# Kernel tuning notes

Hardware: AMD Instinct MI355X
Metric: run time of the kernel (lower is better)

## Reference

```python
import jax, jax.numpy as jnp
import numpy as np

TEMPERATURE = 0.04
EPS = 1e-6

def _conv_valid(x, k, groups=1):
    # x: [N,C,H,W], k: [O,I,kh,kw]
    return jax.lax.conv_general_dilated(
        x, k, window_strides=(1, 1), padding='VALID',
        dimension_numbers=('NCHW', 'OIHW', 'NCHW'),
        feature_group_count=groups)

def setup_inputs() -> dict:
    key = jax.random.key(0)
    k1, k2 = jax.random.split(key)
    roi_piece = jax.random.normal(k1, (256, 1, 17, 17), dtype=jnp.float32)
    roi_background = jax.random.normal(k2, (256, 1, 384, 384), dtype=jnp.float32)
    return {"roi_piece": roi_piece, "roi_background": roi_background}

def reference(roi_piece, roi_background):
    B, _, Ht, Wt = roi_piece.shape
    Hi, Wi = roi_background.shape[-2:]
    Lh, Lw = Hi - Ht + 1, Wi - Wt + 1
    n = Ht * Wt

    # --- template normalization (torch .std is unbiased, ddof=1) ---
    t = roi_piece - jnp.mean(roi_piece, axis=(2, 3), keepdims=True)
    t_std = jnp.maximum(jnp.sqrt(jnp.var(t, axis=(2, 3), keepdims=True, ddof=1)), EPS)
    t_norm = t / t_std  # [B,1,Ht,Wt], zero-mean per batch

    # --- fast ZNCC: since sum(t_norm)==0, corr = corr(image, t_norm) / window_std ---
    # per-batch cross-correlation via grouped conv: batch -> channels/groups
    num = _conv_valid(roi_background.reshape(1, B, Hi, Wi), t_norm, groups=B)[0]  # [B,Lh,Lw]

    # sliding-window mean/var via box filters (var unbiased=False, clamped then sqrt)
    ones_k = jnp.ones((1, 1, Ht, Wt), dtype=roi_background.dtype)
    s1 = _conv_valid(roi_background, ones_k)        # [B,1,Lh,Lw]
    s2 = _conv_valid(roi_background * roi_background, ones_k)
    mu = s1 / n
    var = jnp.maximum(s2 / n - mu * mu, EPS)
    std = jnp.sqrt(var)[:, 0]                        # [B,Lh,Lw]

    corr = num / std  # [B,Lh,Lw]

    # --- soft-argmax over the correlation map ---
    probs = jax.nn.softmax(corr.reshape(B, -1) / TEMPERATURE, axis=-1).reshape(B, Lh, Lw)
    y_coords = jnp.arange(Lh, dtype=corr.dtype)
    x_coords = jnp.arange(Lw, dtype=corr.dtype)
    expected_y = jnp.einsum('bhw,h->b', probs, y_coords)
    expected_x = jnp.einsum('bhw,w->b', probs, x_coords)
    offset_y = expected_y - (Lh - 1) / 2.0
    offset_x = expected_x - (Lw - 1) / 2.0
    offset = jnp.stack([offset_x, offset_y], axis=1)  # [B,2]

    max_corr = jnp.max(corr, axis=(1, 2))             # [B]
    return offset, max_corr
```

## Files before the change

### kernel.cpp

```cpp
#include <hip/hip_runtime.h>
#include <math.h>

#define NB 256
#define HT 17
#define WT 17
#define HI 384
#define WI 384
#define LH 368
#define LW 368
#define NTEMPL 289
#define TPAD 20
#define TY 32
#define TX 128
#define NTXT 3
#define NTYT 12
#define NTILES 36
#define BR 48
#define BP 144
#define TEMP_INV 25.0f
#define EPSV 1e-6f

__global__ __launch_bounds__(256) void tmpl_norm_kernel(
    const float* __restrict__ piece, float* __restrict__ tn) {
    int b = blockIdx.x;
    const float* x = piece + b * NTEMPL;
    int tid = threadIdx.x;
    int wid = tid >> 6, lane = tid & 63;

    float v0 = (tid < NTEMPL) ? x[tid] : 0.f;
    float v1 = (tid + 256 < NTEMPL) ? x[tid + 256] : 0.f;

    __shared__ float sred[4];
    float s = v0 + v1;
    #pragma unroll
    for (int o = 32; o > 0; o >>= 1) s += __shfl_down(s, o, 64);
    if (lane == 0) sred[wid] = s;
    __syncthreads();
    float mean = (sred[0] + sred[1] + sred[2] + sred[3]) * (1.0f / NTEMPL);

    float d0 = (tid < NTEMPL) ? (v0 - mean) : 0.f;
    float d1 = (tid + 256 < NTEMPL) ? (v1 - mean) : 0.f;
    float q = d0 * d0 + d1 * d1;
    __syncthreads();
    #pragma unroll
    for (int o = 32; o > 0; o >>= 1) q += __shfl_down(q, o, 64);
    if (lane == 0) sred[wid] = q;
    __syncthreads();
    float var = (sred[0] + sred[1] + sred[2] + sred[3]) * (1.0f / (NTEMPL - 1));
    float stdv = sqrtf(var);
    if (stdv < EPSV) stdv = EPSV;
    float inv = 1.0f / stdv;

    float* o = tn + b * (HT * TPAD);
    for (int sIdx = tid; sIdx < HT * TPAD; sIdx += 256) {
        int i = sIdx / TPAD, j = sIdx % TPAD;
        o[sIdx] = (j < WT) ? (x[i * WT + j] - mean) * inv : 0.f;
    }
}

template<int P, bool LAST>
__device__ __forceinline__ void corr_step(
    int i, int tr, int xb,
    const float* __restrict__ tp,
    const float (*__restrict__ bg)[BP],
    float (&w)[4][TPAD], float (&tc)[TPAD], float (&acc)[4][4])
{
    const float4* tq = (const float4*)(tp + i * TPAD);
    #pragma unroll
    for (int q = 0; q < 5; ++q) ((float4*)tc)[q] = tq[q];
    #pragma unroll
    for (int j = 0; j < 17; ++j) {
        float tv = tc[j];
        #pragma unroll
        for (int k = 0; k < 4; ++k) acc[0][k] = fmaf(tv, w[P][j + k], acc[0][k]);
    }
    if (!LAST) {
        const float4* br = (const float4*)&bg[tr + i + 4][xb];
        #pragma unroll
        for (int q = 0; q < 5; ++q) ((float4*)w[P])[q] = br[q];
    }
    #pragma unroll
    for (int e = 1; e < 4; ++e) {
        #pragma unroll
        for (int j = 0; j < 17; ++j) {
            float tv = tc[j];
            #pragma unroll
            for (int k = 0; k < 4; ++k)
                acc[e][k] = fmaf(tv, w[(P + e) & 3][j + k], acc[e][k]);
        }
    }
}

template<bool SQ>
__device__ __forceinline__ void build_half(
    const float (*__restrict__ bg)[BP], float (*__restrict__ cb)[BP],
    int r0, int cc)
{
    float s = 0.f;
    #pragma unroll
    for (int i2 = 0; i2 < HT; ++i2) {
        float v = bg[r0 + i2][cc];
        if (SQ) s = fmaf(v, v, s); else s += v;
    }
    cb[0][cc] = s;
    for (int r = 1; r < 16; ++r) {
        float vn = bg[r0 + r + 16][cc], vo = bg[r0 + r - 1][cc];
        if (SQ) s += vn * vn - vo * vo; else s += vn - vo;
        cb[r][cc] = s;
    }
}

__device__ __forceinline__ void consume_half(
    const float (*__restrict__ cb)[BP], int row0, int xb, float (&sv)[4][4])
{
    #pragma unroll
    for (int e = 0; e < 4; ++e) {
        float cf[TPAD];
        const float4* a = (const float4*)&cb[row0 + e][xb];
        #pragma unroll
        for (int q = 0; q < 5; ++q) ((float4*)cf)[q] = a[q];
        float s = 0.f;
        #pragma unroll
        for (int j = 0; j < HT; ++j) s += cf[j];
        sv[e][0] = s;
        #pragma unroll
        for (int k = 1; k < 4; ++k) {
            s += cf[k - 1 + HT] - cf[k - 1];
            sv[e][k] = s;
        }
    }
}

__global__ __launch_bounds__(256, 3) void corr_kernel(
    const float* __restrict__ bgg, const float* __restrict__ tn,
    float* __restrict__ partials) {
    int blk = blockIdx.x;
    int b = blk / NTILES;
    int t = blk % NTILES;
    int ty0 = (t / NTXT) * TY;
    int tx0 = (t % NTXT) * TX;
    const float* img = bgg + (size_t)b * HI * WI;
    const float* tp  = tn + b * (HT * TPAD);

    __shared__ float bg[BR][BP];
    __shared__ float cb[16][BP];
    __shared__ float redm[4], redl[4], redy[4], redx[4];

    int tid = threadIdx.x;
    int wid = tid >> 6, lane = tid & 63;

    for (int l = tid; l < BR * (BP / 4); l += 256) {
        int r = l / (BP / 4), c = (l % (BP / 4)) * 4;
        int iy = ty0 + r, ix = tx0 + c;
        float4 v = make_float4(0.f, 0.f, 0.f, 0.f);
        if (iy < HI && ix < WI) v = *(const float4*)(img + iy * WI + ix);
        *(float4*)&bg[r][c] = v;
    }
    __syncthreads();

    int tr = (tid >> 5) * 4;
    int xb = (tid & 31) * 4;
    float w[4][TPAD];
    float tc[TPAD];
    float acc[4][4] = {};

    #pragma unroll
    for (int m = 0; m < 4; ++m) {
        const float4* br = (const float4*)&bg[tr + m][xb];
        #pragma unroll
        for (int q = 0; q < 5; ++q) ((float4*)w[m])[q] = br[q];
    }

    for (int i = 0; i < 16; i += 4) {
        corr_step<0, false>(i,     tr, xb, tp, bg, w, tc, acc);
        corr_step<1, false>(i + 1, tr, xb, tp, bg, w, tc, acc);
        corr_step<2, false>(i + 2, tr, xb, tp, bg, w, tc, acc);
        corr_step<3, false>(i + 3, tr, xb, tp, bg, w, tc, acc);
    }
    corr_step<0, true>(16, tr, xb, tp, bg, w, tc, acc);

    bool lowHalf = (tr < 16);
    int  row0    = lowHalf ? tr : (tr - 16);
    float s1v[4][4], s2v[4][4];

    if (tid < BP) build_half<false>(bg, cb, 0, tid);
    __syncthreads();
    if (lowHalf) consume_half(cb, row0, xb, s1v);
    __syncthreads();
    if (tid < BP) build_half<false>(bg, cb, 16, tid);
    __syncthreads();
    if (!lowHalf) consume_half(cb, row0, xb, s1v);
    __syncthreads();
    if (tid < BP) build_half<true>(bg, cb, 0, tid);
    __syncthreads();
    if (lowHalf) consume_half(cb, row0, xb, s2v);
    __syncthreads();
    if (tid < BP) build_half<true>(bg, cb, 16, tid);
    __syncthreads();
    if (!lowHalf) consume_half(cb, row0, xb, s2v);

    const float invn = 1.0f / NTEMPL;
    float corr[4][4];
    float m = -INFINITY;
    #pragma unroll
    for (int e = 0; e < 4; ++e) {
        int oy = ty0 + tr + e;
        #pragma unroll
        for (int k = 0; k < 4; ++k) {
            float mu = s1v[e][k] * invn;
            float var = s2v[e][k] * invn - mu * mu;
            if (var < EPSV) var = EPSV;
            float cv = acc[e][k] / sqrtf(var);
            int ox = tx0 + xb + k;
            if (oy < LH && ox < LW) m = fmaxf(m, cv);
            else cv = -INFINITY;
            corr[e][k] = cv;
        }
    }

    float mm = m;
    #pragma unroll
    for (int o = 32; o > 0; o >>= 1) mm = fmaxf(mm, __shfl_down(mm, o, 64));
    if (lane == 0) redm[wid] = mm;
    __syncthreads();
    float M = fmaxf(fmaxf(redm[0], redm[1]), fmaxf(redm[2], redm[3]));

    float l = 0.f, sy = 0.f, sx = 0.f;
    #pragma unroll
    for (int e = 0; e < 4; ++e) {
        int oy = ty0 + tr + e;
        #pragma unroll
        for (int k = 0; k < 4; ++k) {
            float cv = corr[e][k];
            float ev = (cv == -INFINITY) ? 0.f : __expf((cv - M) * TEMP_INV);
            l += ev;
            sy = fmaf(ev, (float)oy, sy);
            sx = fmaf(ev, (float)(tx0 + xb + k), sx);
        }
    }
    #pragma unroll
    for (int o = 32; o > 0; o >>= 1) {
        l  += __shfl_down(l, o, 64);
        sy += __shfl_down(sy, o, 64);
        sx += __shfl_down(sx, o, 64);
    }
    if (lane == 0) { redl[wid] = l; redy[wid] = sy; redx[wid] = sx; }
    __syncthreads();
    if (tid == 0) {
        float* p = partials + (size_t)blk * 4;
        p[0] = M;
        p[1] = redl[0] + redl[1] + redl[2] + redl[3];
        p[2] = redy[0] + redy[1] + redy[2] + redy[3];
        p[3] = redx[0] + redx[1] + redx[2] + redx[3];
    }
}

__global__ __launch_bounds__(256) void reduce_kernel(
    const float* __restrict__ partials, float* __restrict__ out) {
    int b = blockIdx.x;
    int tid = threadIdx.x;
    int wid = tid >> 6, lane = tid & 63;

    float m = -INFINITY, l = 0.f, sy = 0.f, sx = 0.f;
    if (tid < NTILES) {
        const float* p = partials + (size_t)(b * NTILES + tid) * 4;
        m = p[0]; l = p[1]; sy = p[2]; sx = p[3];
    }
    __shared__ float rm[4], rl[4], ry[4], rx[4];
    float mm = m;
    #pragma unroll
    for (int o = 32; o > 0; o >>= 1) mm = fmaxf(mm, __shfl_down(mm, o, 64));
    if (lane == 0) rm[wid] = mm;
    __syncthreads();
    float M = fmaxf(fmaxf(rm[0], rm[1]), fmaxf(rm[2], rm[3]));

    float sc = (m == -INFINITY) ? 0.f : __expf((m - M) * TEMP_INV);
    l *= sc; sy *= sc; sx *= sc;
    #pragma unroll
    for (int o = 32; o > 0; o >>= 1) {
        l  += __shfl_down(l, o, 64);
        sy += __shfl_down(sy, o, 64);
        sx += __shfl_down(sx, o, 64);
    }
    if (lane == 0) { rl[wid] = l; ry[wid] = sy; rx[wid] = sx; }
    __syncthreads();
    if (tid == 0) {
        float L  = rl[0] + rl[1] + rl[2] + rl[3];
        float SY = ry[0] + ry[1] + ry[2] + ry[3];
        float SX = rx[0] + rx[1] + rx[2] + rx[3];
        out[b * 2 + 0] = SX / L - 183.5f;
        out[b * 2 + 1] = SY / L - 183.5f;
        out[2 * NB + b] = M;
    }
}

extern "C" void kernel_launch(void* const* d_in, const int* in_sizes, int n_in,
                              void* d_out, int out_size, void* d_ws, size_t ws_size,
                              hipStream_t stream) {
    const float* piece = (const float*)d_in[0];
    const float* bgg   = (const float*)d_in[1];
    float* out = (float*)d_out;

    float* tn = (float*)d_ws;
    float* partials = tn + NB * HT * TPAD;

    tmpl_norm_kernel<<<NB, 256, 0, stream>>>(piece, tn);
    corr_kernel<<<NB * NTILES, 256, 0, stream>>>(bgg, tn, partials);
    reduce_kernel<<<NB, 256, 0, stream>>>(partials, out);
}
```

Measured before the change: 472.9 us.

## Shrink per-thread row block to three and keep template values in scalar registers

Each thread now computes a 3x4 output block instead of 4x4. The tile shrinks from 32 to 24 rows and the tile count grows from 36 to 48 per batch. The box-filter row partials and rotating window registers are resized to match. Template coefficients are passed through readfirstlane so they live in scalar registers and free vector registers, which should lower VGPR pressure and raise occupancy. The cost is proportionally more halo rows loaded per tile and more blocks overall.

```diff
diff --git a/kernel.cpp b/kernel.cpp
--- a/kernel.cpp
+++ b/kernel.cpp
@@ -10,15 +10,19 @@
 #define LW 368
 #define NTEMPL 289
 #define TPAD 20
-#define TY 32
+#define TY 24
 #define TX 128
 #define NTXT 3
-#define NTYT 12
-#define NTILES 36
-#define BR 48
+#define NTYT 16
+#define NTILES 48
+#define BR 40
 #define BP 144
 #define TEMP_INV 25.0f
 #define EPSV 1e-6f
+
+__device__ __forceinline__ float rfl(float x) {
+    return __int_as_float(__builtin_amdgcn_readfirstlane(__float_as_int(x)));
+}
 
 __global__ __launch_bounds__(256) void tmpl_norm_kernel(
     const float* __restrict__ piece, float* __restrict__ tn) {
@@ -58,35 +62,38 @@
     }
 }
 
-template<int P, bool LAST>
+template<int P, bool PF>
 __device__ __forceinline__ void corr_step(
     int i, int tr, int xb,
     const float* __restrict__ tp,
     const float (*__restrict__ bg)[BP],
-    float (&w)[4][TPAD], float (&tc)[TPAD], float (&acc)[4][4])
+    float (&w)[3][TPAD], float (&acc)[3][4])
 {
+    float tbuf[TPAD];
     const float4* tq = (const float4*)(tp + i * TPAD);
     #pragma unroll
-    for (int q = 0; q < 5; ++q) ((float4*)tc)[q] = tq[q];
+    for (int q = 0; q < 5; ++q) ((float4*)tbuf)[q] = tq[q];
+    float ts[17];
+    #pragma unroll
+    for (int j = 0; j < 17; ++j) ts[j] = rfl(tbuf[j]);
+
     #pragma unroll
     for (int j = 0; j < 17; ++j) {
-        float tv = tc[j];
-        #pragma unroll
-        for (int k = 0; k < 4; ++k) acc[0][k] = fmaf(tv, w[P][j + k], acc[0][k]);
-    }
-    if (!LAST) {
-        const float4* br = (const float4*)&bg[tr + i + 4][xb];
+        #pragma unroll
+        for (int k = 0; k < 4; ++k) acc[0][k] = fmaf(ts[j], w[P][j + k], acc[0][k]);
+    }
+    if (PF) {
+        const float4* br = (const float4*)&bg[tr + i + 3][xb];
         #pragma unroll
         for (int q = 0; q < 5; ++q) ((float4*)w[P])[q] = br[q];
     }
     #pragma unroll
-    for (int e = 1; e < 4; ++e) {
+    for (int e = 1; e < 3; ++e) {
         #pragma unroll
         for (int j = 0; j < 17; ++j) {
-            float tv = tc[j];
             #pragma unroll
             for (int k = 0; k < 4; ++k)
-                acc[e][k] = fmaf(tv, w[(P + e) & 3][j + k], acc[e][k]);
+                acc[e][k] = fmaf(ts[j], w[(P + e) % 3][j + k], acc[e][k]);
         }
     }
 }
@@ -103,7 +110,7 @@
         if (SQ) s = fmaf(v, v, s); else s += v;
     }
     cb[0][cc] = s;
-    for (int r = 1; r < 16; ++r) {
+    for (int r = 1; r < 12; ++r) {
         float vn = bg[r0 + r + 16][cc], vo = bg[r0 + r - 1][cc];
         if (SQ) s += vn * vn - vo * vo; else s += vn - vo;
         cb[r][cc] = s;
@@ -111,10 +118,10 @@
 }
 
 __device__ __forceinline__ void consume_half(
-    const float (*__restrict__ cb)[BP], int row0, int xb, float (&sv)[4][4])
+    const float (*__restrict__ cb)[BP], int row0, int xb, float (&sv)[3][4])
 {
     #pragma unroll
-    for (int e = 0; e < 4; ++e) {
+    for (int e = 0; e < 3; ++e) {
         float cf[TPAD];
         const float4* a = (const float4*)&cb[row0 + e][xb];
         #pragma unroll
@@ -143,7 +150,7 @@
     const float* tp  = tn + b * (HT * TPAD);
 
     __shared__ float bg[BR][BP];
-    __shared__ float cb[16][BP];
+    __shared__ float cb[12][BP];
     __shared__ float redm[4], redl[4], redy[4], redx[4];
 
     int tid = threadIdx.x;
@@ -158,36 +165,35 @@
     }
     __syncthreads();
 
-    int tr = (tid >> 5) * 4;
+    int tr = (tid >> 5) * 3;
     int xb = (tid & 31) * 4;
-    float w[4][TPAD];
-    float tc[TPAD];
-    float acc[4][4] = {};
-
-    #pragma unroll
-    for (int m = 0; m < 4; ++m) {
+    float w[3][TPAD];
+    float acc[3][4] = {};
+
+    #pragma unroll
+    for (int m = 0; m < 3; ++m) {
         const float4* br = (const float4*)&bg[tr + m][xb];
         #pragma unroll
         for (int q = 0; q < 5; ++q) ((float4*)w[m])[q] = br[q];
     }
 
-    for (int i = 0; i < 16; i += 4) {
-        corr_step<0, false>(i,     tr, xb, tp, bg, w, tc, acc);
-        corr_step<1, false>(i + 1, tr, xb, tp, bg, w, tc, acc);
-        corr_step<2, false>(i + 2, tr, xb, tp, bg, w, tc, acc);
-        corr_step<3, false>(i + 3, tr, xb, tp, bg, w, tc, acc);
-    }
-    corr_step<0, true>(16, tr, xb, tp, bg, w, tc, acc);
-
-    bool lowHalf = (tr < 16);
-    int  row0    = lowHalf ? tr : (tr - 16);
-    float s1v[4][4], s2v[4][4];
+    for (int i = 0; i < 15; i += 3) {
+        corr_step<0, true>(i,     tr, xb, tp, bg, w, acc);
+        corr_step<1, true>(i + 1, tr, xb, tp, bg, w, acc);
+        corr_step<2, true>(i + 2, tr, xb, tp, bg, w, acc);
+    }
+    corr_step<0, true >(15, tr, xb, tp, bg, w, acc);
+    corr_step<1, false>(16, tr, xb, tp, bg, w, acc);
+
+    bool lowHalf = (tr < 12);
+    int  row0    = lowHalf ? tr : (tr - 12);
+    float s1v[3][4], s2v[3][4];
 
     if (tid < BP) build_half<false>(bg, cb, 0, tid);
     __syncthreads();
     if (lowHalf) consume_half(cb, row0, xb, s1v);
     __syncthreads();
-    if (tid < BP) build_half<false>(bg, cb, 16, tid);
+    if (tid < BP) build_half<false>(bg, cb, 12, tid);
     __syncthreads();
     if (!lowHalf) consume_half(cb, row0, xb, s1v);
     __syncthreads();
@@ -195,15 +201,15 @@
     __syncthreads();
     if (lowHalf) consume_half(cb, row0, xb, s2v);
     __syncthreads();
-    if (tid < BP) build_half<true>(bg, cb, 16, tid);
+    if (tid < BP) build_half<true>(bg, cb, 12, tid);
     __syncthreads();
     if (!lowHalf) consume_half(cb, row0, xb, s2v);
 
     const float invn = 1.0f / NTEMPL;
-    float corr[4][4];
+    float corr[3][4];
     float m = -INFINITY;
     #pragma unroll
-    for (int e = 0; e < 4; ++e) {
+    for (int e = 0; e < 3; ++e) {
         int oy = ty0 + tr + e;
         #pragma unroll
         for (int k = 0; k < 4; ++k) {
@@ -227,7 +233,7 @@
 
     float l = 0.f, sy = 0.f, sx = 0.f;
     #pragma unroll
-    for (int e = 0; e < 4; ++e) {
+    for (int e = 0; e < 3; ++e) {
         int oy = ty0 + tr + e;
         #pragma unroll
         for (int k = 0; k < 4; ++k) {
```

Result: slower. 485.1 us (+2.6%).

## Load template rows into SGPRs and reshape per-thread tile to 2x8 outputs

Applied to the files above, without the earlier changes.

Template rows are now fetched with scalar loads (s_load_dwordx8) through inline asm, so the broadcast template values sit in scalar registers and no longer take vector registers or LDS/global vector loads. The per-thread output tile changes from 4x4 to 2x8, with 24-wide image row windows and a two-row rolling buffer instead of four. The goal is fewer redundant LDS reads per FMA and lower VGPR pressure. In exchange, the explicit s_waitcnt inside each step can stall the wave, and the wider rows change the LDS access pattern.

```diff
diff --git a/kernel.cpp b/kernel.cpp
--- a/kernel.cpp
+++ b/kernel.cpp
@@ -20,6 +20,18 @@
 #define TEMP_INV 25.0f
 #define EPSV 1e-6f
 
+typedef float f32x8 __attribute__((ext_vector_type(8)));
+
+__device__ __forceinline__ void load_trow_sgpr(
+    const float* p, f32x8& a, f32x8& b, float& c) {
+    asm volatile("s_load_dwordx8 %0, %3, 0x0\n\t"
+                 "s_load_dwordx8 %1, %3, 0x20\n\t"
+                 "s_load_dword %2, %3, 0x40\n\t"
+                 "s_waitcnt lgkmcnt(0)"
+                 : "=&s"(a), "=&s"(b), "=&s"(c)
+                 : "s"(p));
+}
+
 __global__ __launch_bounds__(256) void tmpl_norm_kernel(
     const float* __restrict__ piece, float* __restrict__ tn) {
     int b = blockIdx.x;
@@ -58,36 +70,32 @@
     }
 }
 
-template<int P, bool LAST>
+template<int P, bool PF>
 __device__ __forceinline__ void corr_step(
-    int i, int tr, int xb,
+    int i, int tr2, int xb,
     const float* __restrict__ tp,
     const float (*__restrict__ bg)[BP],
-    float (&w)[4][TPAD], float (&tc)[TPAD], float (&acc)[4][4])
+    float (&w)[2][24], float (&acc)[2][8])
 {
-    const float4* tq = (const float4*)(tp + i * TPAD);
-    #pragma unroll
-    for (int q = 0; q < 5; ++q) ((float4*)tc)[q] = tq[q];
+    f32x8 ta, tb; float tc;
+    load_trow_sgpr(tp + i * TPAD, ta, tb, tc);
+
     #pragma unroll
     for (int j = 0; j < 17; ++j) {
-        float tv = tc[j];
-        #pragma unroll
-        for (int k = 0; k < 4; ++k) acc[0][k] = fmaf(tv, w[P][j + k], acc[0][k]);
-    }
-    if (!LAST) {
-        const float4* br = (const float4*)&bg[tr + i + 4][xb];
-        #pragma unroll
-        for (int q = 0; q < 5; ++q) ((float4*)w[P])[q] = br[q];
-    }
-    #pragma unroll
-    for (int e = 1; e < 4; ++e) {
-        #pragma unroll
-        for (int j = 0; j < 17; ++j) {
-            float tv = tc[j];
-            #pragma unroll
-            for (int k = 0; k < 4; ++k)
-                acc[e][k] = fmaf(tv, w[(P + e) & 3][j + k], acc[e][k]);
-        }
+        float tv = (j < 8) ? ta[j & 7] : (j < 16) ? tb[j & 7] : tc;
+        #pragma unroll
+        for (int k = 0; k < 8; ++k) acc[0][k] = fmaf(tv, w[P][j + k], acc[0][k]);
+    }
+    if (PF) {
+        const float4* br = (const float4*)&bg[tr2 + i + 2][xb];
+        #pragma unroll
+        for (int q = 0; q < 6; ++q) ((float4*)w[P])[q] = br[q];
+    }
+    #pragma unroll
+    for (int j = 0; j < 17; ++j) {
+        float tv = (j < 8) ? ta[j & 7] : (j < 16) ? tb[j & 7] : tc;
+        #pragma unroll
+        for (int k = 0; k < 8; ++k) acc[1][k] = fmaf(tv, w[P ^ 1][j + k], acc[1][k]);
     }
 }
 
@@ -111,20 +119,20 @@
 }
 
 __device__ __forceinline__ void consume_half(
-    const float (*__restrict__ cb)[BP], int row0, int xb, float (&sv)[4][4])
+    const float (*__restrict__ cb)[BP], int row0, int xb, float (&sv)[2][8])
 {
     #pragma unroll
-    for (int e = 0; e < 4; ++e) {
-        float cf[TPAD];
+    for (int e = 0; e < 2; ++e) {
+        float cf[24];
         const float4* a = (const float4*)&cb[row0 + e][xb];
         #pragma unroll
-        for (int q = 0; q < 5; ++q) ((float4*)cf)[q] = a[q];
+        for (int q = 0; q < 6; ++q) ((float4*)cf)[q] = a[q];
         float s = 0.f;
         #pragma unroll
         for (int j = 0; j < HT; ++j) s += cf[j];
         sv[e][0] = s;
         #pragma unroll
-        for (int k = 1; k < 4; ++k) {
+        for (int k = 1; k < 8; ++k) {
             s += cf[k - 1 + HT] - cf[k - 1];
             sv[e][k] = s;
         }
@@ -158,30 +166,27 @@
     }
     __syncthreads();
 
-    int tr = (tid >> 5) * 4;
-    int xb = (tid & 31) * 4;
-    float w[4][TPAD];
-    float tc[TPAD];
-    float acc[4][4] = {};
-
-    #pragma unroll
-    for (int m = 0; m < 4; ++m) {
-        const float4* br = (const float4*)&bg[tr + m][xb];
-        #pragma unroll
-        for (int q = 0; q < 5; ++q) ((float4*)w[m])[q] = br[q];
-    }
-
-    for (int i = 0; i < 16; i += 4) {
-        corr_step<0, false>(i,     tr, xb, tp, bg, w, tc, acc);
-        corr_step<1, false>(i + 1, tr, xb, tp, bg, w, tc, acc);
-        corr_step<2, false>(i + 2, tr, xb, tp, bg, w, tc, acc);
-        corr_step<3, false>(i + 3, tr, xb, tp, bg, w, tc, acc);
-    }
-    corr_step<0, true>(16, tr, xb, tp, bg, w, tc, acc);
-
-    bool lowHalf = (tr < 16);
-    int  row0    = lowHalf ? tr : (tr - 16);
-    float s1v[4][4], s2v[4][4];
+    int tr2 = (tid >> 4) * 2;
+    int xb  = (tid & 15) * 8;
+    float w[2][24];
+    float acc[2][8] = {};
+
+    #pragma unroll
+    for (int m = 0; m < 2; ++m) {
+        const float4* br = (const float4*)&bg[tr2 + m][xb];
+        #pragma unroll
+        for (int q = 0; q < 6; ++q) ((float4*)w[m])[q] = br[q];
+    }
+
+    for (int i = 0; i < 16; i += 2) {
+        corr_step<0, true>(i,     tr2, xb, tp, bg, w, acc);
+        corr_step<1, true>(i + 1, tr2, xb, tp, bg, w, acc);
+    }
+    corr_step<0, false>(16, tr2, xb, tp, bg, w, acc);
+
+    bool lowHalf = (tr2 < 16);
+    int  row0    = lowHalf ? tr2 : (tr2 - 16);
+    float s1v[2][8], s2v[2][8];
 
     if (tid < BP) build_half<false>(bg, cb, 0, tid);
     __syncthreads();
@@ -200,13 +205,13 @@
     if (!lowHalf) consume_half(cb, row0, xb, s2v);
 
     const float invn = 1.0f / NTEMPL;
-    float corr[4][4];
+    float corr[2][8];
     float m = -INFINITY;
     #pragma unroll
-    for (int e = 0; e < 4; ++e) {
-        int oy = ty0 + tr + e;
-        #pragma unroll
-        for (int k = 0; k < 4; ++k) {
+    for (int e = 0; e < 2; ++e) {
+        int oy = ty0 + tr2 + e;
+        #pragma unroll
+        for (int k = 0; k < 8; ++k) {
             float mu = s1v[e][k] * invn;
             float var = s2v[e][k] * invn - mu * mu;
             if (var < EPSV) var = EPSV;
@@ -227,10 +232,10 @@
 
     float l = 0.f, sy = 0.f, sx = 0.f;
     #pragma unroll
-    for (int e = 0; e < 4; ++e) {
-        int oy = ty0 + tr + e;
-        #pragma unroll
-        for (int k = 0; k < 4; ++k) {
+    for (int e = 0; e < 2; ++e) {
+        int oy = ty0 + tr2 + e;
+        #pragma unroll
+        for (int k = 0; k < 8; ++k) {
             float cv = corr[e][k];
             float ev = (cv == -INFINITY) ? 0.f : __expf((cv - M) * TEMP_INV);
             l += ev;
```

Result: no change. 473.0 us (+0.0%).
